# Optimization experiments

Measured on AMD Instinct MI355X. Metric: run time of the kernel, lower is better.

## Reference

```python
import jax, jax.numpy as jnp
import numpy as np

BATCH = 16384
N_FEAT = 2048
SWAP_PROB = 0.1


def setup_inputs() -> dict:
    key = jax.random.key(0)
    k_x, k_mask, k_perm = jax.random.split(key, 3)
    x = jax.random.normal(k_x, (BATCH, N_FEAT), dtype=jnp.float32)
    # swap_mask[i, j] = True with prob swap_prob (matches torch.rand(...) < swap_prob)
    swap_mask = jax.random.uniform(k_mask, (BATCH, N_FEAT)) < SWAP_PROB
    # per-row random permutation (matches torch.randperm per batch row),
    # vectorized as argsort of iid uniforms
    perm = jnp.argsort(jax.random.uniform(k_perm, (BATCH, N_FEAT)), axis=1).astype(jnp.int32)
    return {"x": x, "swap_mask": swap_mask, "perm": perm}


def reference(x, swap_mask, perm):
    # x[i, swap_mask[i]] = x[i, perm[i][swap_mask[i]]]  (vectorized over rows)
    swapped = jnp.take_along_axis(x, perm, axis=1)  # [B, F]
    return jnp.where(swap_mask, swapped, x)
```

## Files before the change

kernel.cpp:

```cpp
#include <hip/hip_runtime.h>

#define NFEAT 2048
#define BATCH 16384

typedef float v4f __attribute__((ext_vector_type(4)));

__global__ __launch_bounds__(256) void swap_corrupt_kernel(
    const float* __restrict__ x,
    const int*   __restrict__ mask,
    const int*   __restrict__ perm,
    float*       __restrict__ out)
{
    const int r = blockIdx.x;
    const int t = threadIdx.x;
    const size_t base = (size_t)r * NFEAT;

    const float4* __restrict__ x4 = (const float4*)(x + base);
    const int4*   __restrict__ m4 = (const int4*)(mask + base);
    const int4*   __restrict__ p4 = (const int4*)(perm + base);
    const float*  __restrict__ xr = x + base;

    float4 a  = x4[t];
    float4 b  = x4[t + 256];
    int4   m0 = m4[t];
    int4   m1 = m4[t + 256];
    int4   p0 = p4[t];
    int4   p1 = p4[t + 256];

    v4f* __restrict__ o4 = (v4f*)(out + base);

    {
        v4f o;
        o.x = m0.x ? xr[p0.x] : a.x;
        o.y = m0.y ? xr[p0.y] : a.y;
        o.z = m0.z ? xr[p0.z] : a.z;
        o.w = m0.w ? xr[p0.w] : a.w;
        __builtin_nontemporal_store(o, &o4[t]);
    }
    {
        v4f o;
        o.x = m1.x ? xr[p1.x] : b.x;
        o.y = m1.y ? xr[p1.y] : b.y;
        o.z = m1.z ? xr[p1.z] : b.z;
        o.w = m1.w ? xr[p1.w] : b.w;
        __builtin_nontemporal_store(o, &o4[t + 256]);
    }
}

extern "C" void kernel_launch(void* const* d_in, const int* in_sizes, int n_in,
                              void* d_out, int out_size, void* d_ws, size_t ws_size,
                              hipStream_t stream) {
    const float* x    = (const float*)d_in[0];
    const int*   mask = (const int*)d_in[1];
    const int*   perm = (const int*)d_in[2];
    float*       out  = (float*)d_out;

    swap_corrupt_kernel<<<dim3(BATCH), dim3(256), 0, stream>>>(x, mask, perm, out);
}
```

Before: 386.6 us.

## Use persistent grid-stride blocks with register double-buffered row prefetch

Launches a fixed grid of 2048 blocks, each handling 8 rows in a grid-stride loop. The next row's x, mask and perm vectors are loaded into registers while the current row's gathers and stores are issued, so streaming loads overlap the dependent gather latency. The cost is higher register use per thread and fewer resident waves, and fewer blocks may leave less latency hiding from occupancy.

New measurement: 393.4 us. No clear change (+1.8%).

```diff
diff --git a/kernel.cpp b/kernel.cpp
--- a/kernel.cpp
+++ b/kernel.cpp
@@ -2,8 +2,50 @@
 
 #define NFEAT 2048
 #define BATCH 16384
+#define GRID  2048
 
 typedef float v4f __attribute__((ext_vector_type(4)));
+
+struct RowRegs { float4 a, b; int4 m0, m1, p0, p1; };
+
+__device__ __forceinline__ void load_row(const float* __restrict__ x,
+                                         const int* __restrict__ mask,
+                                         const int* __restrict__ perm,
+                                         int r, int t, RowRegs& R)
+{
+    const size_t base = (size_t)r * NFEAT;
+    const float4* __restrict__ x4 = (const float4*)(x + base);
+    const int4*   __restrict__ m4 = (const int4*)(mask + base);
+    const int4*   __restrict__ p4 = (const int4*)(perm + base);
+    R.a  = x4[t];       R.b  = x4[t + 256];
+    R.m0 = m4[t];       R.m1 = m4[t + 256];
+    R.p0 = p4[t];       R.p1 = p4[t + 256];
+}
+
+__device__ __forceinline__ void proc_row(const float* __restrict__ x,
+                                         float* __restrict__ out,
+                                         int r, int t, const RowRegs& R)
+{
+    const size_t base = (size_t)r * NFEAT;
+    const float* __restrict__ xr = x + base;
+    v4f* __restrict__ o4 = (v4f*)(out + base);
+    {
+        v4f o;
+        o.x = R.m0.x ? xr[R.p0.x] : R.a.x;
+        o.y = R.m0.y ? xr[R.p0.y] : R.a.y;
+        o.z = R.m0.z ? xr[R.p0.z] : R.a.z;
+        o.w = R.m0.w ? xr[R.p0.w] : R.a.w;
+        __builtin_nontemporal_store(o, &o4[t]);
+    }
+    {
+        v4f o;
+        o.x = R.m1.x ? xr[R.p1.x] : R.b.x;
+        o.y = R.m1.y ? xr[R.p1.y] : R.b.y;
+        o.z = R.m1.z ? xr[R.p1.z] : R.b.z;
+        o.w = R.m1.w ? xr[R.p1.w] : R.b.w;
+        __builtin_nontemporal_store(o, &o4[t + 256]);
+    }
+}
 
 __global__ __launch_bounds__(256) void swap_corrupt_kernel(
     const float* __restrict__ x,
@@ -11,40 +53,19 @@
     const int*   __restrict__ perm,
     float*       __restrict__ out)
 {
-    const int r = blockIdx.x;
     const int t = threadIdx.x;
-    const size_t base = (size_t)r * NFEAT;
+    int r = blockIdx.x;
 
-    const float4* __restrict__ x4 = (const float4*)(x + base);
-    const int4*   __restrict__ m4 = (const int4*)(mask + base);
-    const int4*   __restrict__ p4 = (const int4*)(perm + base);
-    const float*  __restrict__ xr = x + base;
+    RowRegs cur, nxt;
+    load_row(x, mask, perm, r, t, cur);
 
-    float4 a  = x4[t];
-    float4 b  = x4[t + 256];
-    int4   m0 = m4[t];
-    int4   m1 = m4[t + 256];
-    int4   p0 = p4[t];
-    int4   p1 = p4[t + 256];
-
-    v4f* __restrict__ o4 = (v4f*)(out + base);
-
-    {
-        v4f o;
-        o.x = m0.x ? xr[p0.x] : a.x;
-        o.y = m0.y ? xr[p0.y] : a.y;
-        o.z = m0.z ? xr[p0.z] : a.z;
-        o.w = m0.w ? xr[p0.w] : a.w;
-        __builtin_nontemporal_store(o, &o4[t]);
+    for (int rn = r + GRID; rn < BATCH; rn += GRID) {
+        load_row(x, mask, perm, rn, t, nxt);
+        proc_row(x, out, r, t, cur);
+        cur = nxt;
+        r = rn;
     }
-    {
-        v4f o;
-        o.x = m1.x ? xr[p1.x] : b.x;
-        o.y = m1.y ? xr[p1.y] : b.y;
-        o.z = m1.z ? xr[p1.z] : b.z;
-        o.w = m1.w ? xr[p1.w] : b.w;
-        __builtin_nontemporal_store(o, &o4[t + 256]);
-    }
+    proc_row(x, out, r, t, cur);
 }
 
 extern "C" void kernel_launch(void* const* d_in, const int* in_sizes, int n_in,
@@ -55,5 +76,5 @@
     const int*   perm = (const int*)d_in[2];
     float*       out  = (float*)d_out;
 
-    swap_corrupt_kernel<<<dim3(BATCH), dim3(256), 0, stream>>>(x, mask, perm, out);
+    swap_corrupt_kernel<<<dim3(GRID), dim3(256), 0, stream>>>(x, mask, perm, out);
 }
```
